# Kernel tuning notes

Measured on AMD Instinct MI355X. Metric: run time of the kernel, lower is better.

The kernel has to match this reference:

```python
import jax, jax.numpy as jnp
import numpy as np


def setup_inputs() -> dict:
    key = jax.random.key(0)
    k1, k2, k3 = jax.random.split(key, 3)
    B, C, H, W = 4, 16, 64, 64
    F, K = 32, 3
    x = jax.random.normal(k1, (B, C, H, W), dtype=jnp.float32)
    # Pade coefficients per (out_channel, in_channel, a, b): numerator deg 5, denom deg 4.
    nums = jax.random.normal(k2, (F, C, K, K, 6), dtype=jnp.float32) * 0.3
    denoms = jax.random.normal(k3, (F, C, K, K, 4), dtype=jnp.float32) * 0.3
    return {"x": x, "nums": nums, "denoms": denoms}


def _rational_conv(x, nums, denoms):
    B, C, H, W = x.shape
    F, _, K, _, _ = nums.shape
    p = (K - 1) // 2
    # pad spatially, move channels last: (B, H+2p, W+2p, C)
    xp = jnp.pad(x, ((0, 0), (0, 0), (p, p), (p, p))).transpose(0, 2, 3, 1)
    # im2col patches: stack the K*K shifted views -> (B, H, W, K2, C)
    patches = jnp.stack(
        [xp[:, a:a + H, b:b + W, :] for a in range(K) for b in range(K)], axis=3
    )
    # powers x^0..x^5 built by repeated multiply (safe for negative bases)
    pws = [jnp.ones_like(patches)]
    for _ in range(5):
        pws.append(pws[-1] * patches)
    pw = jnp.stack(pws, axis=-1)                         # (B,H,W,K2,C,6)
    nums_r = nums.reshape(F, C, K * K, 6)                # (a,b) flattened a*K+b, matches patch order
    denoms_r = denoms.reshape(F, C, K * K, 4)
    # P(x) = sum_n a_n x^n ; Q(x) = 1 + |sum_m b_m x^m|, m=1..4  (Pade version A)
    P = jnp.einsum('bhwkcn,fckn->bhwfkc', pw, nums_r)
    Q = 1.0 + jnp.abs(jnp.einsum('bhwkcm,fckm->bhwfkc', pw[..., 1:5], denoms_r))
    out = (P / Q).sum(axis=(4, 5))                       # (B,H,W,F)
    return out.transpose(0, 3, 1, 2)                     # (B,F,H,W)


def reference(x, nums, denoms):
    return _rational_conv(x, nums, denoms)
```

## Files before the change

kernel.cpp:

```cpp
#include <hip/hip_runtime.h>

#define B_ 4
#define C_ 16
#define H_ 64
#define W_ 64
#define F_ 32
#define S_ 66
#define CH_ (S_ * S_)
#define NPAD_ (B_ * C_ * CH_)
#define CST 12

__global__ __launch_bounds__(256)
void pad_kernel(const float* __restrict__ x, float* __restrict__ xp) {
    const int i  = blockIdx.x * 256 + threadIdx.x;
    const int cc = i % S_;
    const int t  = i / S_;
    const int r  = t % S_;
    const int bc = t / S_;
    float v = 0.f;
    if (r >= 1 && r <= H_ && cc >= 1 && cc <= W_)
        v = x[(size_t)bc * (H_ * W_) + (r - 1) * W_ + (cc - 1)];
    xp[i] = v;
}

__global__ __launch_bounds__(256)
void ka_rconv_kernel(const float* __restrict__ xp,
                     const float* __restrict__ nums,
                     const float* __restrict__ denoms,
                     float* __restrict__ out) {
    __shared__ alignas(16) float sc[C_ * 9 * CST];
    __shared__ float red[3 * 4 * 64];

    const int tid = threadIdx.x;
    const int col = tid & 63;
    const int wg  = tid >> 6;

    int bid = blockIdx.x;
    const int f  = bid & 31;  bid >>= 5;
    const int t4 = bid & 15;  bid >>= 4;
    const int b  = bid;
    const int gy0 = t4 * 4;

    {
        const float* np = nums + (size_t)f * (C_ * 54);
        for (int i = tid; i < C_ * 54; i += 256) {
            int e = i / 6, j = i - e * 6;
            sc[e * CST + j] = np[i];
        }
        const float* dp = denoms + (size_t)f * (C_ * 36);
        for (int i = tid; i < C_ * 36; i += 256) {
            int e = i / 4, j = i - e * 4;
            sc[e * CST + 6 + j] = dp[i];
        }
    }
    __syncthreads();

    const int chb = __builtin_amdgcn_readfirstlane(wg * 4);
    const float* xb = xp + ((size_t)(b * C_ + chb)) * CH_ + gy0 * S_ + col;
    const float* cp = sc + chb * (9 * CST);

    float acc[4] = {0.f, 0.f, 0.f, 0.f};

    for (int c = 0; c < 4; ++c) {
        const float* xr = xb + c * CH_;
        float3 rv[6];
        #pragma unroll
        for (int k = 0; k < 6; ++k)
            rv[k] = *(const float3*)(xr + k * S_);

        const float* ce = cp + c * (9 * CST);
        #pragma unroll
        for (int t = 0; t < 9; ++t) {
            const float4 k0 = *(const float4*)(ce + t * CST);
            const float4 k1 = *(const float4*)(ce + t * CST + 4);
            const float2 k2 = *(const float2*)(ce + t * CST + 8);
            const int a = t / 3, j = t % 3;
            #pragma unroll
            for (int p = 0; p < 4; ++p) {
                const float3 r3 = rv[p + a];
                const float xv = (j == 0) ? r3.x : (j == 1) ? r3.y : r3.z;

                float P = fmaf(k1.y, xv, k1.x);
                P = fmaf(P, xv, k0.w);
                P = fmaf(P, xv, k0.z);
                P = fmaf(P, xv, k0.y);
                P = fmaf(P, xv, k0.x);

                float Q = fmaf(k2.y, xv, k2.x);
                Q = fmaf(Q, xv, k1.w);
                Q = fmaf(Q, xv, k1.z);
                Q *= xv;
                Q = 1.0f + fabsf(Q);

                acc[p] = fmaf(P, __builtin_amdgcn_rcpf(Q), acc[p]);
            }
        }
    }

    if (wg > 0) {
        #pragma unroll
        for (int p = 0; p < 4; ++p)
            red[((wg - 1) * 4 + p) * 64 + col] = acc[p];
    }
    __syncthreads();
    if (wg == 0) {
        float* op = out + (((size_t)b * F_ + f) * H_ + gy0) * W_ + col;
        #pragma unroll
        for (int p = 0; p < 4; ++p) {
            float s = acc[p] + red[(0 * 4 + p) * 64 + col]
                             + red[(1 * 4 + p) * 64 + col]
                             + red[(2 * 4 + p) * 64 + col];
            op[p * W_] = s;
        }
    }
}

extern "C" void kernel_launch(void* const* d_in, const int* in_sizes, int n_in,
                              void* d_out, int out_size, void* d_ws, size_t ws_size,
                              hipStream_t stream) {
    const float* x      = (const float*)d_in[0];
    const float* nums   = (const float*)d_in[1];
    const float* denoms = (const float*)d_in[2];
    float* outp = (float*)d_out;
    float* xpad = (float*)d_ws;

    pad_kernel<<<NPAD_ / 256, 256, 0, stream>>>(x, xpad);
    dim3 grid(B_ * 16 * F_);
    ka_rconv_kernel<<<grid, 256, 0, stream>>>(xpad, nums, denoms, outp);
}
```

Baseline: 83.52 us.

## Pack input and coefficients into half2 channel pairs and evaluate rationals in packed fp16

```diff
diff --git a/kernel.cpp b/kernel.cpp
--- a/kernel.cpp
+++ b/kernel.cpp
@@ -1,4 +1,5 @@
 #include <hip/hip_runtime.h>
+#include <hip/hip_fp16.h>
 
 #define B_ 4
 #define C_ 16
@@ -6,29 +7,58 @@
 #define W_ 64
 #define F_ 32
 #define S_ 66
-#define CH_ (S_ * S_)
-#define NPAD_ (B_ * C_ * CH_)
-#define CST 12
+#define CHW_ (S_ * S_)
+#define XN_ (B_ * 8 * CHW_)
+#define CN_ (F_ * 8 * 9 * 12)
+#define CSTRIDE 12
+
+typedef _Float16 hvec2 __attribute__((ext_vector_type(2)));
 
 __global__ __launch_bounds__(256)
-void pad_kernel(const float* __restrict__ x, float* __restrict__ xp) {
-    const int i  = blockIdx.x * 256 + threadIdx.x;
+void pack_x_kernel(const float* __restrict__ x, __half2* __restrict__ xw) {
+    const int i = blockIdx.x * 256 + threadIdx.x;
+    if (i >= XN_) return;
     const int cc = i % S_;
-    const int t  = i / S_;
+    int t = i / S_;
     const int r  = t % S_;
-    const int bc = t / S_;
-    float v = 0.f;
-    if (r >= 1 && r <= H_ && cc >= 1 && cc <= W_)
-        v = x[(size_t)bc * (H_ * W_) + (r - 1) * W_ + (cc - 1)];
-    xp[i] = v;
+    t /= S_;
+    const int pr = t % 8;
+    const int b  = t / 8;
+    float lo = 0.f, hi = 0.f;
+    if (r >= 1 && r <= H_ && cc >= 1 && cc <= W_) {
+        const int sp = (r - 1) * W_ + (cc - 1);
+        lo = x[((size_t)(b * C_ + pr)     ) * (H_ * W_) + sp];
+        hi = x[((size_t)(b * C_ + pr + 8)) * (H_ * W_) + sp];
+    }
+    xw[i] = __halves2half2(__float2half_rn(lo), __float2half_rn(hi));
 }
 
 __global__ __launch_bounds__(256)
-void ka_rconv_kernel(const float* __restrict__ xp,
-                     const float* __restrict__ nums,
-                     const float* __restrict__ denoms,
+void pack_coef_kernel(const float* __restrict__ nums, const float* __restrict__ denoms,
+                      __half2* __restrict__ cw) {
+    const int i = blockIdx.x * 256 + threadIdx.x;
+    if (i >= F_ * 8 * 9) return;
+    const int tap = i % 9;
+    const int pr  = (i / 9) % 8;
+    const int f   = i / 72;
+    __half2* o = cw + (size_t)i * CSTRIDE;
+    const size_t nlo = (((size_t)f * C_ + pr)     * 9 + tap) * 6;
+    const size_t nhi = (((size_t)f * C_ + pr + 8) * 9 + tap) * 6;
+    for (int k = 0; k < 6; ++k)
+        o[k] = __halves2half2(__float2half_rn(nums[nlo + k]), __float2half_rn(nums[nhi + k]));
+    const size_t dlo = (((size_t)f * C_ + pr)     * 9 + tap) * 4;
+    const size_t dhi = (((size_t)f * C_ + pr + 8) * 9 + tap) * 4;
+    for (int k = 0; k < 4; ++k)
+        o[6 + k] = __halves2half2(__float2half_rn(denoms[dlo + k]), __float2half_rn(denoms[dhi + k]));
+    o[10] = __halves2half2(__half(0.f), __half(0.f));
+    o[11] = o[10];
+}
+
+__global__ __launch_bounds__(256)
+void ka_rconv_kernel(const __half2* __restrict__ xw,
+                     const __half2* __restrict__ cw,
                      float* __restrict__ out) {
-    __shared__ alignas(16) float sc[C_ * 9 * CST];
+    __shared__ __half2 sc[8 * 9 * CSTRIDE];
     __shared__ float red[3 * 4 * 64];
 
     const int tid = threadIdx.x;
@@ -41,58 +71,57 @@
     const int b  = bid;
     const int gy0 = t4 * 4;
 
-    {
-        const float* np = nums + (size_t)f * (C_ * 54);
-        for (int i = tid; i < C_ * 54; i += 256) {
-            int e = i / 6, j = i - e * 6;
-            sc[e * CST + j] = np[i];
-        }
-        const float* dp = denoms + (size_t)f * (C_ * 36);
-        for (int i = tid; i < C_ * 36; i += 256) {
-            int e = i / 4, j = i - e * 4;
-            sc[e * CST + 6 + j] = dp[i];
-        }
-    }
+    for (int i = tid; i < 8 * 9 * CSTRIDE; i += 256)
+        sc[i] = cw[(size_t)f * (8 * 9 * CSTRIDE) + i];
     __syncthreads();
 
-    const int chb = __builtin_amdgcn_readfirstlane(wg * 4);
-    const float* xb = xp + ((size_t)(b * C_ + chb)) * CH_ + gy0 * S_ + col;
-    const float* cp = sc + chb * (9 * CST);
-
+    const __half2 one = __halves2half2(__half(1.0f), __half(1.0f));
     float acc[4] = {0.f, 0.f, 0.f, 0.f};
 
-    for (int c = 0; c < 4; ++c) {
-        const float* xr = xb + c * CH_;
-        float3 rv[6];
+    for (int cp = 0; cp < 2; ++cp) {
+        const int pr = __builtin_amdgcn_readfirstlane(wg * 2 + cp);
+        const __half2* xbase = xw + ((size_t)(b * 8 + pr) * S_ + gy0) * S_ + col;
+
+        uint3 rv[6];
         #pragma unroll
         for (int k = 0; k < 6; ++k)
-            rv[k] = *(const float3*)(xr + k * S_);
+            rv[k] = *(const uint3*)(xbase + k * S_);
 
-        const float* ce = cp + c * (9 * CST);
+        const __half2* ce = sc + pr * (9 * CSTRIDE);
         #pragma unroll
         for (int t = 0; t < 9; ++t) {
-            const float4 k0 = *(const float4*)(ce + t * CST);
-            const float4 k1 = *(const float4*)(ce + t * CST + 4);
-            const float2 k2 = *(const float2*)(ce + t * CST + 8);
+            const __half2 n0 = ce[t*CSTRIDE+0], n1 = ce[t*CSTRIDE+1], n2 = ce[t*CSTRIDE+2];
+            const __half2 n3 = ce[t*CSTRIDE+3], n4 = ce[t*CSTRIDE+4], n5 = ce[t*CSTRIDE+5];
+            const __half2 d0 = ce[t*CSTRIDE+6], d1 = ce[t*CSTRIDE+7];
+            const __half2 d2 = ce[t*CSTRIDE+8], d3 = ce[t*CSTRIDE+9];
             const int a = t / 3, j = t % 3;
             #pragma unroll
             for (int p = 0; p < 4; ++p) {
-                const float3 r3 = rv[p + a];
-                const float xv = (j == 0) ? r3.x : (j == 1) ? r3.y : r3.z;
+                const uint3 r3 = rv[p + a];
+                const unsigned u = (j == 0) ? r3.x : (j == 1) ? r3.y : r3.z;
+                const __half2 xp = __builtin_bit_cast(__half2, u);
 
-                float P = fmaf(k1.y, xv, k1.x);
-                P = fmaf(P, xv, k0.w);
-                P = fmaf(P, xv, k0.z);
-                P = fmaf(P, xv, k0.y);
-                P = fmaf(P, xv, k0.x);
+                __half2 P = __hfma2(n5, xp, n4);
+                P = __hfma2(P, xp, n3);
+                P = __hfma2(P, xp, n2);
+                P = __hfma2(P, xp, n1);
+                P = __hfma2(P, xp, n0);
 
-                float Q = fmaf(k2.y, xv, k2.x);
-                Q = fmaf(Q, xv, k1.w);
-                Q = fmaf(Q, xv, k1.z);
-                Q *= xv;
-                Q = 1.0f + fabsf(Q);
+                __half2 Sd = __hfma2(d3, xp, d2);
+                Sd = __hfma2(Sd, xp, d1);
+                Sd = __hfma2(Sd, xp, d0);
+                Sd = __hmul2(Sd, xp);
 
-                acc[p] = fmaf(P, __builtin_amdgcn_rcpf(Q), acc[p]);
+                const __half2 Q = __hadd2(one, __habs2(Sd));
+                const __half2 R = h2rcp(Q);
+#if __has_builtin(__builtin_amdgcn_fdot2)
+                acc[p] = __builtin_amdgcn_fdot2(__builtin_bit_cast(hvec2, P),
+                                                __builtin_bit_cast(hvec2, R),
+                                                acc[p], false);
+#else
+                const __half2 PR = __hmul2(P, R);
+                acc[p] += __low2float(PR) + __high2float(PR);
+#endif
             }
         }
     }
@@ -122,9 +151,11 @@
     const float* nums   = (const float*)d_in[1];
     const float* denoms = (const float*)d_in[2];
     float* outp = (float*)d_out;
-    float* xpad = (float*)d_ws;
+    __half2* xw = (__half2*)d_ws;
+    __half2* cwp = xw + XN_;
 
-    pad_kernel<<<NPAD_ / 256, 256, 0, stream>>>(x, xpad);
+    pack_x_kernel<<<(XN_ + 255) / 256, 256, 0, stream>>>(x, xw);
+    pack_coef_kernel<<<(F_ * 8 * 9 + 255) / 256, 256, 0, stream>>>(nums, denoms, cwp);
     dim3 grid(B_ * 16 * F_);
-    ka_rconv_kernel<<<grid, 256, 0, stream>>>(xpad, nums, denoms, outp);
+    ka_rconv_kernel<<<grid, 256, 0, stream>>>(xw, cwp, outp);
 }
```

Measured after the change: 80.96 us. -3.1%, faster.
